# Kernel tuning notes

Measured on AMD Instinct MI355X. Metric: run time of the kernel, lower is better.

## Reference

```python
import jax, jax.numpy as jnp
import numpy as np

WS = (8, 8)          # window_size
ITER = 1             # iterations
QK_SCALE = 0.17677669529663687  # 32**-0.5


def _l2norm(x, eps=1e-12):
    n = jnp.linalg.norm(x, axis=-1, keepdims=True)
    return x / jnp.maximum(n, eps)


def _get_mask(H, W, onehot, gain=1.0):
    # onehot: [B, h, L, S] cluster assignment weights
    coords = jnp.stack(jnp.meshgrid(jnp.arange(H), jnp.arange(W), indexing='ij'))
    coords = coords.reshape(2, -1).astype(jnp.float32)  # [2, L]
    s = jnp.sum(onehot, axis=-2, keepdims=True)         # [B, h, 1, S]
    s = jnp.where(s == 0, 1.0, s)
    centers = jnp.einsum('cl,bhls->bhcs', coords, onehot) / s  # [B, h, 2, S]
    dh = coords[0][None, None, :, None] - centers[:, :, 0, None, :]  # [B,h,L,S]
    dw = coords[1][None, None, :, None] - centers[:, :, 1, None, :]
    dist = jnp.sqrt(dh * dh + dw * dw)
    return jnp.exp(-dist) * gain  # 1/exp(d) * gain


def setup_inputs() -> dict:
    key = jax.random.key(0)
    k1, k2 = jax.random.split(key)
    B, h, H, W, d = 8, 8, 64, 64, 32
    x_k = jax.random.normal(k1, (B, h, H, W, d), dtype=jnp.float32)
    x_v = jax.random.normal(k2, (B, h, H, W, d), dtype=jnp.float32)
    scale = jnp.asarray(1.0, dtype=jnp.float32)  # nn.Parameter init value
    return {"x_k": x_k, "x_v": x_v, "scale": scale}


def reference(x_k, x_v, scale):
    B, h, H, W, d = x_k.shape
    ws0, ws1 = WS
    H_, W_ = H // ws0, W // ws1
    L, L_ = H * W, H_ * W_

    # initCenter: average pool over non-overlapping windows, then L2 normalize (q only)
    c_q = x_k.reshape(B, h, H_, ws0, W_, ws1, d).mean(axis=(3, 5)).reshape(B, h, L_, d)
    c_q = _l2norm(c_q)

    # initRPE: each pixel assigned to its window index -> one-hot -> coordinate mask
    win_idx = (jnp.arange(H)[:, None] // ws0) * W_ + jnp.arange(W)[None, :] // ws1  # [H, W]
    onehot0 = jax.nn.one_hot(win_idx.reshape(-1), L_, dtype=jnp.float32)[None, None]  # [1,1,L,L_]
    rpb = jnp.broadcast_to(_get_mask(H, W, onehot0), (B, h, L, L_))
    rpb = jax.lax.stop_gradient(rpb)

    xf = x_k.reshape(B, h, L, d)
    aff = None
    for _ in range(ITER):
        # updateCenter: scaled affinity + bias, hard-max mask, softmax, weighted sum, renorm
        aff = jnp.einsum('bhld,bhmd->bhlm', xf * (QK_SCALE * scale), c_q) + rpb
        mx = jnp.max(aff, axis=-1, keepdims=True)
        aff = jax.nn.softmax(jnp.where(aff < mx, -jnp.inf, aff), axis=-1)
        c_q = _l2norm(jnp.einsum('bhlm,bhld->bhmd', aff, xf))
        rpb = jax.lax.stop_gradient(_get_mask(H, W, aff))

    c_v_sum = jnp.einsum('bhlm,bhld->bhmd', aff, x_v.reshape(B, h, L, d))
    a_sum = jnp.sum(aff, axis=-2)[..., None]  # [B, h, L_, 1]
    a_sum = jnp.where(a_sum == 0, 1.0, a_sum)
    c_v = c_v_sum / a_sum
    return (c_q, c_v, rpb)
```

## Files before the change

### kernel.cpp

```cpp
#include <hip/hip_runtime.h>
#include <math.h>


#define NMAPS   64
#define LPIX    4096
#define NCLUS   64
#define DIM     32
#define CHUNKS  8
#define PSTRIDE 4288

__global__ __launch_bounds__(256) void k_initcenter(const float* __restrict__ xk,
                                                    float* __restrict__ cq0) {
    int wid  = threadIdx.x >> 6;
    int lane = threadIdx.x & 63;
    int c    = blockIdx.x * 4 + wid;
    int bh   = c >> 6, m = c & 63;
    int wh   = m >> 3, wc = m & 7;
    int d    = lane & 31, half = lane >> 5;
    const float* base = xk + (size_t)bh * LPIX * DIM;
    float s = 0.f;
#pragma unroll
    for (int k = 0; k < 32; ++k) {
        int pix = k * 2 + half;
        int r = pix >> 3, cc = pix & 7;
        int row = wh * 8 + r, col = wc * 8 + cc;
        s += base[((row << 6) + col) * DIM + d];
    }
    s += __shfl_xor(s, 32);
    float ss = s * s;
#pragma unroll
    for (int o = 16; o >= 1; o >>= 1) ss += __shfl_xor(ss, o);
    float mean = s * (1.0f / 64.0f);
    float norm = sqrtf(ss) * (1.0f / 64.0f);
    float inv  = 1.0f / fmaxf(norm, 1e-12f);
    if (half == 0) cq0[(size_t)c * DIM + d] = mean * inv;
}

__global__ __launch_bounds__(256) void k_assign(const float* __restrict__ xk,
                                                const float* __restrict__ xv,
                                                const float* __restrict__ scale,
                                                const float* __restrict__ cq0,
                                                float* __restrict__ partial) {
    __shared__ float cs[NCLUS * DIM];
    __shared__ float aq[NCLUS * 33];
    __shared__ float av[NCLUS * 33];
    __shared__ float as_[NCLUS], ach[NCLUS], acw[NCLUS];

    int t     = threadIdx.x;
    int bh    = blockIdx.x >> 3;
    int chunk = blockIdx.x & (CHUNKS - 1);

#pragma unroll
    for (int i = 0; i < 8; ++i) cs[t + i * 256] = cq0[(size_t)bh * 2048 + t + i * 256];
    for (int i = t; i < NCLUS * 33; i += 256) { aq[i] = 0.f; av[i] = 0.f; }
    if (t < NCLUS) { as_[t] = 0.f; ach[t] = 0.f; acw[t] = 0.f; }
    __syncthreads();

    float qs = 0.17677669529663687f * scale[0];
    const float* xkb = xk + (size_t)bh * LPIX * DIM;
    const float* xvb = xv + (size_t)bh * LPIX * DIM;

    for (int pp = 0; pp < 2; ++pp) {
        int l = chunk * 512 + pp * 256 + t;
        float fi = (float)(l >> 6);
        float fj = (float)(l & 63);

        float xr[DIM];
        const float4* xp = (const float4*)(xkb + (size_t)l * DIM);
#pragma unroll
        for (int k = 0; k < 8; ++k) {
            float4 v = xp[k];
            xr[k*4] = v.x; xr[k*4+1] = v.y; xr[k*4+2] = v.z; xr[k*4+3] = v.w;
        }

        float mx = -INFINITY;
        unsigned long long msk = 0ull;
        for (int m = 0; m < NCLUS; ++m) {
            const float4* cm4 = (const float4*)&cs[m * DIM];
            float dot = 0.f;
#pragma unroll
            for (int k = 0; k < 8; ++k) {
                float4 c4 = cm4[k];
                dot = fmaf(xr[k*4],   c4.x, dot);
                dot = fmaf(xr[k*4+1], c4.y, dot);
                dot = fmaf(xr[k*4+2], c4.z, dot);
                dot = fmaf(xr[k*4+3], c4.w, dot);
            }
            float dh = fi - (float)((m >> 3) * 8) - 3.5f;
            float dw = fj - (float)((m & 7) * 8) - 3.5f;
            float rp = expf(-sqrtf(fmaf(dh, dh, dw * dw)));
            float val = fmaf(dot, qs, rp);
            if (val > mx)       { mx = val; msk = 1ull << m; }
            else if (val == mx) { msk |= 1ull << m; }
        }
        float w = 1.0f / (float)__popcll(msk);

        float vr[DIM];
        const float4* vp = (const float4*)(xvb + (size_t)l * DIM);
#pragma unroll
        for (int k = 0; k < 8; ++k) {
            float4 v = vp[k];
            vr[k*4] = v.x; vr[k*4+1] = v.y; vr[k*4+2] = v.z; vr[k*4+3] = v.w;
        }

        while (msk) {
            int m = __builtin_ctzll(msk);
            msk &= msk - 1;
            float* aqm = &aq[m * 33];
            float* avm = &av[m * 33];
#pragma unroll
            for (int d = 0; d < DIM; ++d) {
                atomicAdd(&aqm[d], w * xr[d]);
                atomicAdd(&avm[d], w * vr[d]);
            }
            atomicAdd(&as_[m], w);
            atomicAdd(&ach[m], w * fi);
            atomicAdd(&acw[m], w * fj);
        }
    }
    __syncthreads();

    float* pw = partial + (size_t)blockIdx.x * PSTRIDE;
    for (int i = t; i < 2048; i += 256) {
        pw[i]        = aq[(i >> 5) * 33 + (i & 31)];
        pw[2048 + i] = av[(i >> 5) * 33 + (i & 31)];
    }
    if (t < NCLUS) {
        pw[4096 + t] = as_[t];
        pw[4160 + t] = ach[t];
        pw[4224 + t] = acw[t];
    }
}

__global__ __launch_bounds__(256) void k_reduce(const float* __restrict__ partial,
                                                float* __restrict__ out,
                                                float* __restrict__ cen) {
    __shared__ float sk[2048], sv[2048];
    __shared__ float ss_[NCLUS], sch[NCLUS], scw[NCLUS];
    __shared__ float invq[NCLUS], invv[NCLUS];
    int bh = blockIdx.x, t = threadIdx.x;
    const float* pw = partial + (size_t)bh * CHUNKS * PSTRIDE;

    for (int i = t; i < 2048; i += 256) {
        float a = 0.f, b = 0.f;
#pragma unroll
        for (int p = 0; p < CHUNKS; ++p) {
            a += pw[(size_t)p * PSTRIDE + i];
            b += pw[(size_t)p * PSTRIDE + 2048 + i];
        }
        sk[i] = a; sv[i] = b;
    }
    if (t < NCLUS) {
        float a = 0.f, b = 0.f, c = 0.f;
#pragma unroll
        for (int p = 0; p < CHUNKS; ++p) {
            a += pw[(size_t)p * PSTRIDE + 4096 + t];
            b += pw[(size_t)p * PSTRIDE + 4160 + t];
            c += pw[(size_t)p * PSTRIDE + 4224 + t];
        }
        ss_[t] = a; sch[t] = b; scw[t] = c;
    }
    __syncthreads();
    if (t < NCLUS) {
        float s2 = 0.f;
#pragma unroll
        for (int d = 0; d < DIM; ++d) { float v = sk[t * DIM + d]; s2 = fmaf(v, v, s2); }
        invq[t] = 1.0f / fmaxf(sqrtf(s2), 1e-12f);
        float s  = ss_[t];
        float sp = (s == 0.f) ? 1.f : s;
        invv[t] = 1.0f / sp;
        cen[bh * NCLUS + t]        = sch[t] / sp;
        cen[4096 + bh * NCLUS + t] = scw[t] / sp;
    }
    __syncthreads();
    float* cq = out;
    float* cv = out + 131072;
    for (int i = t; i < 2048; i += 256) {
        int m = i >> 5;
        cq[(size_t)bh * 2048 + i] = sk[i] * invq[m];
        cv[(size_t)bh * 2048 + i] = sv[i] * invv[m];
    }
}

__global__ __launch_bounds__(256) void k_rpb(const float* __restrict__ cen,
                                             float* __restrict__ out) {
    size_t g = (size_t)blockIdx.x * 256 + threadIdx.x;
    int m      = (int)(g & 63);
    size_t lbh = g >> 6;
    int l  = (int)(lbh & 4095);
    int bh = (int)(lbh >> 12);
    float fi = (float)(l >> 6);
    float fj = (float)(l & 63);
    float ch = cen[bh * NCLUS + m];
    float cw = cen[4096 + bh * NCLUS + m];
    float dh = fi - ch, dw = fj - cw;
    out[262144 + g] = expf(-sqrtf(fmaf(dh, dh, dw * dw)));
}

extern "C" void kernel_launch(void* const* d_in, const int* in_sizes, int n_in,
                              void* d_out, int out_size, void* d_ws, size_t ws_size,
                              hipStream_t stream) {
    const float* xk    = (const float*)d_in[0];
    const float* xv    = (const float*)d_in[1];
    const float* scale = (const float*)d_in[2];
    float* out = (float*)d_out;
    float* ws  = (float*)d_ws;

    float* cq0     = ws;
    float* cen     = ws + 131072;
    float* partial = ws + 139264;

    k_initcenter<<<1024, 256, 0, stream>>>(xk, cq0);
    k_assign<<<NMAPS * CHUNKS, 256, 0, stream>>>(xk, xv, scale, cq0, partial);
    k_reduce<<<NMAPS, 256, 0, stream>>>(partial, out, cen);
    k_rpb<<<65536, 256, 0, stream>>>(cen, out);
}
```

Baseline: 265.2 us.

## Precompute initial RPE table, read centers from global, widen assign blocks, replicate accumulators

After: 250.7 us. -5.4%, faster.

```diff
diff --git a/kernel.cpp b/kernel.cpp
--- a/kernel.cpp
+++ b/kernel.cpp
@@ -36,99 +36,111 @@
     if (half == 0) cq0[(size_t)c * DIM + d] = mean * inv;
 }
 
-__global__ __launch_bounds__(256) void k_assign(const float* __restrict__ xk,
+__global__ __launch_bounds__(256) void k_rpe0(float* __restrict__ rp0) {
+    int g = blockIdx.x * 256 + threadIdx.x;
+    int m = g & 63, l = g >> 6;
+    float fi = (float)(l >> 6);
+    float fj = (float)(l & 63);
+    float dh = fi - (float)((m >> 3) * 8) - 3.5f;
+    float dw = fj - (float)((m & 7) * 8) - 3.5f;
+    rp0[g] = expf(-sqrtf(fmaf(dh, dh, dw * dw)));
+}
+
+__global__ __launch_bounds__(512) void k_assign(const float* __restrict__ xk,
                                                 const float* __restrict__ xv,
                                                 const float* __restrict__ scale,
                                                 const float* __restrict__ cq0,
+                                                const float* __restrict__ rp0,
                                                 float* __restrict__ partial) {
-    __shared__ float cs[NCLUS * DIM];
-    __shared__ float aq[NCLUS * 33];
-    __shared__ float av[NCLUS * 33];
-    __shared__ float as_[NCLUS], ach[NCLUS], acw[NCLUS];
+    __shared__ float aq[2][NCLUS * 33];
+    __shared__ float av[2][NCLUS * 33];
+    __shared__ float as_[2][NCLUS], ach[2][NCLUS], acw[2][NCLUS];
 
     int t     = threadIdx.x;
     int bh    = blockIdx.x >> 3;
     int chunk = blockIdx.x & (CHUNKS - 1);
 
-#pragma unroll
-    for (int i = 0; i < 8; ++i) cs[t + i * 256] = cq0[(size_t)bh * 2048 + t + i * 256];
-    for (int i = t; i < NCLUS * 33; i += 256) { aq[i] = 0.f; av[i] = 0.f; }
-    if (t < NCLUS) { as_[t] = 0.f; ach[t] = 0.f; acw[t] = 0.f; }
+    {
+        float* aqf = &aq[0][0];
+        float* avf = &av[0][0];
+        for (int i = t; i < 2 * NCLUS * 33; i += 512) { aqf[i] = 0.f; avf[i] = 0.f; }
+        if (t < 2 * NCLUS) { (&as_[0][0])[t] = 0.f; (&ach[0][0])[t] = 0.f; (&acw[0][0])[t] = 0.f; }
+    }
     __syncthreads();
 
     float qs = 0.17677669529663687f * scale[0];
+    const float* cqb = cq0 + (size_t)bh * 2048;
     const float* xkb = xk + (size_t)bh * LPIX * DIM;
     const float* xvb = xv + (size_t)bh * LPIX * DIM;
 
-    for (int pp = 0; pp < 2; ++pp) {
-        int l = chunk * 512 + pp * 256 + t;
-        float fi = (float)(l >> 6);
-        float fj = (float)(l & 63);
-
-        float xr[DIM];
-        const float4* xp = (const float4*)(xkb + (size_t)l * DIM);
-#pragma unroll
-        for (int k = 0; k < 8; ++k) {
-            float4 v = xp[k];
-            xr[k*4] = v.x; xr[k*4+1] = v.y; xr[k*4+2] = v.z; xr[k*4+3] = v.w;
-        }
-
-        float mx = -INFINITY;
-        unsigned long long msk = 0ull;
-        for (int m = 0; m < NCLUS; ++m) {
-            const float4* cm4 = (const float4*)&cs[m * DIM];
+    int l = chunk * 512 + t;
+    float fi = (float)(l >> 6);
+    float fj = (float)(l & 63);
+
+    float xr[DIM];
+    const float4* xp = (const float4*)(xkb + (size_t)l * DIM);
+#pragma unroll
+    for (int k = 0; k < 8; ++k) {
+        float4 v = xp[k];
+        xr[k*4] = v.x; xr[k*4+1] = v.y; xr[k*4+2] = v.z; xr[k*4+3] = v.w;
+    }
+
+    const float4* rpl = (const float4*)(rp0 + (size_t)l * 64);
+    float mx = -INFINITY;
+    unsigned long long msk = 0ull;
+#pragma unroll
+    for (int m4 = 0; m4 < 16; ++m4) {
+        float4 r4 = rpl[m4];
+        float rj[4] = {r4.x, r4.y, r4.z, r4.w};
+#pragma unroll
+        for (int j = 0; j < 4; ++j) {
+            int m = m4 * 4 + j;
+            const float* cm = cqb + m * DIM;
             float dot = 0.f;
 #pragma unroll
-            for (int k = 0; k < 8; ++k) {
-                float4 c4 = cm4[k];
-                dot = fmaf(xr[k*4],   c4.x, dot);
-                dot = fmaf(xr[k*4+1], c4.y, dot);
-                dot = fmaf(xr[k*4+2], c4.z, dot);
-                dot = fmaf(xr[k*4+3], c4.w, dot);
-            }
-            float dh = fi - (float)((m >> 3) * 8) - 3.5f;
-            float dw = fj - (float)((m & 7) * 8) - 3.5f;
-            float rp = expf(-sqrtf(fmaf(dh, dh, dw * dw)));
-            float val = fmaf(dot, qs, rp);
+            for (int k = 0; k < DIM; ++k) dot = fmaf(xr[k], cm[k], dot);
+            float val = fmaf(dot, qs, rj[j]);
             if (val > mx)       { mx = val; msk = 1ull << m; }
             else if (val == mx) { msk |= 1ull << m; }
         }
-        float w = 1.0f / (float)__popcll(msk);
-
-        float vr[DIM];
-        const float4* vp = (const float4*)(xvb + (size_t)l * DIM);
-#pragma unroll
-        for (int k = 0; k < 8; ++k) {
-            float4 v = vp[k];
-            vr[k*4] = v.x; vr[k*4+1] = v.y; vr[k*4+2] = v.z; vr[k*4+3] = v.w;
-        }
-
-        while (msk) {
-            int m = __builtin_ctzll(msk);
-            msk &= msk - 1;
-            float* aqm = &aq[m * 33];
-            float* avm = &av[m * 33];
-#pragma unroll
-            for (int d = 0; d < DIM; ++d) {
-                atomicAdd(&aqm[d], w * xr[d]);
-                atomicAdd(&avm[d], w * vr[d]);
-            }
-            atomicAdd(&as_[m], w);
-            atomicAdd(&ach[m], w * fi);
-            atomicAdd(&acw[m], w * fj);
-        }
+    }
+    float w = 1.0f / (float)__popcll(msk);
+
+    float vr[DIM];
+    const float4* vp = (const float4*)(xvb + (size_t)l * DIM);
+#pragma unroll
+    for (int k = 0; k < 8; ++k) {
+        float4 v = vp[k];
+        vr[k*4] = v.x; vr[k*4+1] = v.y; vr[k*4+2] = v.z; vr[k*4+3] = v.w;
+    }
+
+    int rep = t & 1;
+    while (msk) {
+        int m = __builtin_ctzll(msk);
+        msk &= msk - 1;
+        float* aqm = &aq[rep][m * 33];
+        float* avm = &av[rep][m * 33];
+#pragma unroll
+        for (int d = 0; d < DIM; ++d) {
+            atomicAdd(&aqm[d], w * xr[d]);
+            atomicAdd(&avm[d], w * vr[d]);
+        }
+        atomicAdd(&as_[rep][m], w);
+        atomicAdd(&ach[rep][m], w * fi);
+        atomicAdd(&acw[rep][m], w * fj);
     }
     __syncthreads();
 
     float* pw = partial + (size_t)blockIdx.x * PSTRIDE;
-    for (int i = t; i < 2048; i += 256) {
-        pw[i]        = aq[(i >> 5) * 33 + (i & 31)];
-        pw[2048 + i] = av[(i >> 5) * 33 + (i & 31)];
+    for (int i = t; i < 2048; i += 512) {
+        int s = (i >> 5) * 33 + (i & 31);
+        pw[i]        = aq[0][s] + aq[1][s];
+        pw[2048 + i] = av[0][s] + av[1][s];
     }
     if (t < NCLUS) {
-        pw[4096 + t] = as_[t];
-        pw[4160 + t] = ach[t];
-        pw[4224 + t] = acw[t];
+        pw[4096 + t] = as_[0][t] + as_[1][t];
+        pw[4160 + t] = ach[0][t] + ach[1][t];
+        pw[4224 + t] = acw[0][t] + acw[1][t];
     }
 }
 
@@ -209,9 +221,11 @@
     float* cq0     = ws;
     float* cen     = ws + 131072;
     float* partial = ws + 139264;
+    float* rp0     = ws + 139264 + 512 * PSTRIDE;
 
     k_initcenter<<<1024, 256, 0, stream>>>(xk, cq0);
-    k_assign<<<NMAPS * CHUNKS, 256, 0, stream>>>(xk, xv, scale, cq0, partial);
+    k_rpe0<<<1024, 256, 0, stream>>>(rp0);
+    k_assign<<<NMAPS * CHUNKS, 512, 0, stream>>>(xk, xv, scale, cq0, rp0, partial);
     k_reduce<<<NMAPS, 256, 0, stream>>>(partial, out, cen);
     k_rpb<<<65536, 256, 0, stream>>>(cen, out);
 }
```

## Precompute initial RPE table, double assign chunks, vectorize rpb writes

Applied to the files above, without the earlier changes.

New measurement: 242.7 us. 8.5% less time.

```diff
diff --git a/kernel.cpp b/kernel.cpp
--- a/kernel.cpp
+++ b/kernel.cpp
@@ -6,11 +6,12 @@
 #define LPIX    4096
 #define NCLUS   64
 #define DIM     32
-#define CHUNKS  8
+#define CHUNKS  16
 #define PSTRIDE 4288
 
 __global__ __launch_bounds__(256) void k_initcenter(const float* __restrict__ xk,
-                                                    float* __restrict__ cq0) {
+                                                    float* __restrict__ cq0,
+                                                    float* __restrict__ rp0) {
     int wid  = threadIdx.x >> 6;
     int lane = threadIdx.x & 63;
     int c    = blockIdx.x * 4 + wid;
@@ -34,12 +35,21 @@
     float norm = sqrtf(ss) * (1.0f / 64.0f);
     float inv  = 1.0f / fmaxf(norm, 1e-12f);
     if (half == 0) cq0[(size_t)c * DIM + d] = mean * inv;
+
+    int g  = blockIdx.x * 256 + threadIdx.x;
+    int mm = g & 63, l = g >> 6;
+    float fi = (float)(l >> 6);
+    float fj = (float)(l & 63);
+    float dh = fi - (float)((mm >> 3) * 8) - 3.5f;
+    float dw = fj - (float)((mm & 7) * 8) - 3.5f;
+    rp0[g] = expf(-sqrtf(fmaf(dh, dh, dw * dw)));
 }
 
 __global__ __launch_bounds__(256) void k_assign(const float* __restrict__ xk,
                                                 const float* __restrict__ xv,
                                                 const float* __restrict__ scale,
                                                 const float* __restrict__ cq0,
+                                                const float* __restrict__ rp0,
                                                 float* __restrict__ partial) {
     __shared__ float cs[NCLUS * DIM];
     __shared__ float aq[NCLUS * 33];
@@ -47,7 +57,7 @@
     __shared__ float as_[NCLUS], ach[NCLUS], acw[NCLUS];
 
     int t     = threadIdx.x;
-    int bh    = blockIdx.x >> 3;
+    int bh    = blockIdx.x >> 4;
     int chunk = blockIdx.x & (CHUNKS - 1);
 
 #pragma unroll
@@ -60,22 +70,28 @@
     const float* xkb = xk + (size_t)bh * LPIX * DIM;
     const float* xvb = xv + (size_t)bh * LPIX * DIM;
 
-    for (int pp = 0; pp < 2; ++pp) {
-        int l = chunk * 512 + pp * 256 + t;
-        float fi = (float)(l >> 6);
-        float fj = (float)(l & 63);
-
-        float xr[DIM];
-        const float4* xp = (const float4*)(xkb + (size_t)l * DIM);
-#pragma unroll
-        for (int k = 0; k < 8; ++k) {
-            float4 v = xp[k];
-            xr[k*4] = v.x; xr[k*4+1] = v.y; xr[k*4+2] = v.z; xr[k*4+3] = v.w;
-        }
-
-        float mx = -INFINITY;
-        unsigned long long msk = 0ull;
-        for (int m = 0; m < NCLUS; ++m) {
+    int l = chunk * 256 + t;
+    float fi = (float)(l >> 6);
+    float fj = (float)(l & 63);
+
+    float xr[DIM];
+    const float4* xp = (const float4*)(xkb + (size_t)l * DIM);
+#pragma unroll
+    for (int k = 0; k < 8; ++k) {
+        float4 v = xp[k];
+        xr[k*4] = v.x; xr[k*4+1] = v.y; xr[k*4+2] = v.z; xr[k*4+3] = v.w;
+    }
+
+    const float4* rpl = (const float4*)(rp0 + (size_t)l * 64);
+    float mx = -INFINITY;
+    unsigned long long msk = 0ull;
+#pragma unroll
+    for (int m4 = 0; m4 < 16; ++m4) {
+        float4 r4 = rpl[m4];
+        float rj[4] = {r4.x, r4.y, r4.z, r4.w};
+#pragma unroll
+        for (int j = 0; j < 4; ++j) {
+            int m = m4 * 4 + j;
             const float4* cm4 = (const float4*)&cs[m * DIM];
             float dot = 0.f;
 #pragma unroll
@@ -86,44 +102,42 @@
                 dot = fmaf(xr[k*4+2], c4.z, dot);
                 dot = fmaf(xr[k*4+3], c4.w, dot);
             }
-            float dh = fi - (float)((m >> 3) * 8) - 3.5f;
-            float dw = fj - (float)((m & 7) * 8) - 3.5f;
-            float rp = expf(-sqrtf(fmaf(dh, dh, dw * dw)));
-            float val = fmaf(dot, qs, rp);
+            float val = fmaf(dot, qs, rj[j]);
             if (val > mx)       { mx = val; msk = 1ull << m; }
             else if (val == mx) { msk |= 1ull << m; }
         }
-        float w = 1.0f / (float)__popcll(msk);
-
-        float vr[DIM];
-        const float4* vp = (const float4*)(xvb + (size_t)l * DIM);
-#pragma unroll
-        for (int k = 0; k < 8; ++k) {
-            float4 v = vp[k];
-            vr[k*4] = v.x; vr[k*4+1] = v.y; vr[k*4+2] = v.z; vr[k*4+3] = v.w;
-        }
-
-        while (msk) {
-            int m = __builtin_ctzll(msk);
-            msk &= msk - 1;
-            float* aqm = &aq[m * 33];
-            float* avm = &av[m * 33];
-#pragma unroll
-            for (int d = 0; d < DIM; ++d) {
-                atomicAdd(&aqm[d], w * xr[d]);
-                atomicAdd(&avm[d], w * vr[d]);
-            }
-            atomicAdd(&as_[m], w);
-            atomicAdd(&ach[m], w * fi);
-            atomicAdd(&acw[m], w * fj);
-        }
+    }
+    float w = 1.0f / (float)__popcll(msk);
+
+    float vr[DIM];
+    const float4* vp = (const float4*)(xvb + (size_t)l * DIM);
+#pragma unroll
+    for (int k = 0; k < 8; ++k) {
+        float4 v = vp[k];
+        vr[k*4] = v.x; vr[k*4+1] = v.y; vr[k*4+2] = v.z; vr[k*4+3] = v.w;
+    }
+
+    while (msk) {
+        int m = __builtin_ctzll(msk);
+        msk &= msk - 1;
+        float* aqm = &aq[m * 33];
+        float* avm = &av[m * 33];
+#pragma unroll
+        for (int d = 0; d < DIM; ++d) {
+            atomicAdd(&aqm[d], w * xr[d]);
+            atomicAdd(&avm[d], w * vr[d]);
+        }
+        atomicAdd(&as_[m], w);
+        atomicAdd(&ach[m], w * fi);
+        atomicAdd(&acw[m], w * fj);
     }
     __syncthreads();
 
     float* pw = partial + (size_t)blockIdx.x * PSTRIDE;
     for (int i = t; i < 2048; i += 256) {
-        pw[i]        = aq[(i >> 5) * 33 + (i & 31)];
-        pw[2048 + i] = av[(i >> 5) * 33 + (i & 31)];
+        int sidx = (i >> 5) * 33 + (i & 31);
+        pw[i]        = aq[sidx];
+        pw[2048 + i] = av[sidx];
     }
     if (t < NCLUS) {
         pw[4096 + t] = as_[t];
@@ -184,17 +198,21 @@
 
 __global__ __launch_bounds__(256) void k_rpb(const float* __restrict__ cen,
                                              float* __restrict__ out) {
-    size_t g = (size_t)blockIdx.x * 256 + threadIdx.x;
-    int m      = (int)(g & 63);
-    size_t lbh = g >> 6;
-    int l  = (int)(lbh & 4095);
-    int bh = (int)(lbh >> 12);
+    int g4 = blockIdx.x * 256 + threadIdx.x;
+    int mg = (g4 & 15) * 4;
+    int lbh = g4 >> 4;
+    int l  = lbh & 4095;
+    int bh = lbh >> 12;
     float fi = (float)(l >> 6);
     float fj = (float)(l & 63);
-    float ch = cen[bh * NCLUS + m];
-    float cw = cen[4096 + bh * NCLUS + m];
-    float dh = fi - ch, dw = fj - cw;
-    out[262144 + g] = expf(-sqrtf(fmaf(dh, dh, dw * dw)));
+    float4 ch4 = *(const float4*)&cen[bh * 64 + mg];
+    float4 cw4 = *(const float4*)&cen[4096 + bh * 64 + mg];
+    float4 o;
+    { float dh = fi - ch4.x, dw = fj - cw4.x; o.x = expf(-sqrtf(fmaf(dh, dh, dw * dw))); }
+    { float dh = fi - ch4.y, dw = fj - cw4.y; o.y = expf(-sqrtf(fmaf(dh, dh, dw * dw))); }
+    { float dh = fi - ch4.z, dw = fj - cw4.z; o.z = expf(-sqrtf(fmaf(dh, dh, dw * dw))); }
+    { float dh = fi - ch4.w, dw = fj - cw4.w; o.w = expf(-sqrtf(fmaf(dh, dh, dw * dw))); }
+    *(float4*)&out[262144 + (size_t)g4 * 4] = o;
 }
 
 extern "C" void kernel_launch(void* const* d_in, const int* in_sizes, int n_in,
@@ -209,9 +227,10 @@
     float* cq0     = ws;
     float* cen     = ws + 131072;
     float* partial = ws + 139264;
-
-    k_initcenter<<<1024, 256, 0, stream>>>(xk, cq0);
-    k_assign<<<NMAPS * CHUNKS, 256, 0, stream>>>(xk, xv, scale, cq0, partial);
+    float* rp0     = ws + 139264 + 1024 * PSTRIDE;
+
+    k_initcenter<<<1024, 256, 0, stream>>>(xk, cq0, rp0);
+    k_assign<<<NMAPS * CHUNKS, 256, 0, stream>>>(xk, xv, scale, cq0, rp0, partial);
     k_reduce<<<NMAPS, 256, 0, stream>>>(partial, out, cen);
-    k_rpb<<<65536, 256, 0, stream>>>(cen, out);
-}
+    k_rpb<<<16384, 256, 0, stream>>>(cen, out);
+}
```
